# Kernel tuning notes

Measured on AMD Instinct MI355X. Metric: run time of the kernel, lower is better.

## Reference

```python
import jax, jax.numpy as jnp
import numpy as np

B, S, TRG, SRC2 = 64, 2048, 512, 1024  # batch, src_len, trg_hidden, 2*src_hidden


def setup_inputs() -> dict:
    key = jax.random.key(0)
    ks = jax.random.split(key, 9)
    return {
        "dehy": jax.random.normal(ks[0], (B, TRG), dtype=jnp.float32),
        "enhy": jax.random.normal(ks[1], (B, S, SRC2), dtype=jnp.float32),
        "past_attn": jax.random.uniform(ks[2], (B, S), dtype=jnp.float32),
        "src_mask": jax.random.randint(ks[3], (B, S), 0, 2, dtype=jnp.int32),
        # parameters (torch Linear: y = x @ W.T + b)
        "W_en": jax.random.normal(ks[4], (TRG, SRC2), dtype=jnp.float32) * 0.02,
        "b_en": jnp.zeros((TRG,), dtype=jnp.float32),
        "W_de": jax.random.normal(ks[5], (TRG, TRG), dtype=jnp.float32) * 0.02,
        "w_cv": jax.random.normal(ks[6], (TRG,), dtype=jnp.float32) * 0.02,   # attn_cv_in: Linear(1, trg)
        "w_warp": jax.random.normal(ks[7], (TRG,), dtype=jnp.float32) * 0.02, # attn_warp_in: Linear(trg, 1)
    }


def reference(dehy, enhy, past_attn, src_mask, W_en, b_en, W_de, w_cv, w_warp):
    # luong_concat score with 'asee' coverage term
    # attn_agg: [B, S, TRG]
    attn_agg = (
        jnp.einsum("bsd,hd->bsh", enhy, W_en) + b_en
        + (dehy @ W_de.T)[:, None, :]
        + past_attn[..., None] * w_cv
    )
    attn_agg = jnp.tanh(attn_agg)
    attn_ee = jnp.einsum("bsh,h->bs", attn_agg, w_warp)  # [B, S]
    # masked_fill(|mask| == 0, -1e20)
    attn_ee = jnp.where(jnp.abs(src_mask) == 0, jnp.float32(-1e20), attn_ee)
    attn = jax.nn.softmax(attn_ee, axis=1)
    c_encoder = jnp.einsum("bs,bsd->bd", attn, enhy)  # [B, SRC2]
    return (c_encoder, attn, attn_ee)
```

## Files before the change

kernel.cpp:

```cpp
#include <hip/hip_runtime.h>

#define B_   64
#define S_   2048
#define TRG_ 512
#define K_   1024

typedef short short8 __attribute__((ext_vector_type(8)));
typedef float f32x4  __attribute__((ext_vector_type(4)));
typedef unsigned short us4 __attribute__((ext_vector_type(4)));

__device__ __forceinline__ unsigned short f2bf(float f) {
    union { float f; unsigned int u; } v; v.f = f;
    unsigned int u = v.u;
    unsigned int r = (u + 0x7fffu + ((u >> 16) & 1u)) >> 16;
    return (unsigned short)r;
}

__global__ void wen_convert_kernel(const float* __restrict__ Wen,
                                   unsigned short* __restrict__ Wbf) {
    int idx = blockIdx.x * 256 + threadIdx.x;
    float4 f = ((const float4*)Wen)[idx];
    us4 o = { f2bf(f.x), f2bf(f.y), f2bf(f.z), f2bf(f.w) };
    ((us4*)Wbf)[idx] = o;
}

__global__ void deproj_kernel(const float* __restrict__ dehy,
                              const float* __restrict__ Wde,
                              const float* __restrict__ ben,
                              float* __restrict__ dp) {
    int b = blockIdx.x >> 1;
    int h = ((blockIdx.x & 1) << 8) + threadIdx.x;
    const float4* dv = (const float4*)(dehy + (size_t)b * TRG_);
    const float4* wv = (const float4*)(Wde + (size_t)h * TRG_);
    float s = ben[h];
    #pragma unroll 4
    for (int t = 0; t < TRG_ / 4; ++t) {
        float4 a = dv[t], w = wv[t];
        s += a.x * w.x + a.y * w.y + a.z * w.z + a.w * w.w;
    }
    dp[b * TRG_ + h] = s;
}

__global__ __launch_bounds__(512, 2) void score_kernel(
    const float* __restrict__ enhy,
    const unsigned short* __restrict__ Wbf,
    const float* __restrict__ dp,
    const float* __restrict__ past_attn,
    const int* __restrict__ src_mask,
    const float* __restrict__ w_cv,
    const float* __restrict__ w_warp,
    float* __restrict__ out_ee)
{
    __shared__ unsigned short Abuf[2][128 * 32];
    __shared__ unsigned short Bbuf[2][512 * 32];
    __shared__ float red[4][128];

    const int tid  = threadIdx.x;
    const int lane = tid & 63;
    const int w    = tid >> 6;
    const int wm   = w >> 2;
    const int wn   = w & 3;
    const int lj   = lane & 15;
    const int lg   = lane >> 4;
    const int m0   = blockIdx.x * 128;
    const int b    = m0 >> 11;
    const int s0   = m0 & 2047;

    const int kx = ((lg ^ (lane & 3)) << 4);

    f32x4 acc[4][8];
    const f32x4 fz = {0.f, 0.f, 0.f, 0.f};
    #pragma unroll
    for (int i = 0; i < 4; ++i)
        #pragma unroll
        for (int j = 0; j < 8; ++j) acc[i][j] = fz;

    const int arow = tid >> 2;
    const int achk = tid & 3;
    const float* aSrc = enhy + (size_t)(m0 + arow) * K_ + (achk << 3);
    const int aDstByte = arow * 64 + ((achk ^ (arow & 3)) << 4);

    const unsigned short* bSrc[4];
    unsigned short* bDst[4];
    #pragma unroll
    for (int j = 0; j < 4; ++j) {
        int cp = (j << 9) + tid;
        int brow = cp >> 2, bkc = cp & 3;
        bSrc[j] = Wbf + (size_t)brow * K_ + ((bkc ^ (brow & 3)) << 3);
        bDst[j] = &Bbuf[0][0] + ((j << 9) + (w << 6)) * 8;
    }

    float4 a0, a1;
    auto load_a = [&](int kt) {
        const float* p = aSrc + kt * 32;
        a0 = *(const float4*)p;
        a1 = *(const float4*)(p + 4);
    };
    auto write_a = [&](int bufsel) {
        short8 v;
        v[0] = (short)f2bf(a0.x); v[1] = (short)f2bf(a0.y);
        v[2] = (short)f2bf(a0.z); v[3] = (short)f2bf(a0.w);
        v[4] = (short)f2bf(a1.x); v[5] = (short)f2bf(a1.y);
        v[6] = (short)f2bf(a1.z); v[7] = (short)f2bf(a1.w);
        *(short8*)((char*)&Abuf[bufsel][0] + aDstByte) = v;
    };
    auto stage_b = [&](int bufsel, int kt) {
        #pragma unroll
        for (int j = 0; j < 4; ++j) {
            __builtin_amdgcn_global_load_lds(
                (const __attribute__((address_space(1))) void*)(bSrc[j] + kt * 32),
                (__attribute__((address_space(3))) void*)(bDst[j] + bufsel * (512 * 32)),
                16, 0, 0);
        }
    };
    auto compute = [&](int bufsel) {
        const char* Bbase = (const char*)&Bbuf[bufsel][0];
        const char* Abase = (const char*)&Abuf[bufsel][0];
        short8 bf[8];
        #pragma unroll
        for (int fn = 0; fn < 8; ++fn) {
            int r = (wn << 7) + (fn << 4) + lj;
            bf[fn] = *(const short8*)(Bbase + r * 64 + kx);
        }
        #pragma unroll
        for (int fm = 0; fm < 4; ++fm) {
            int rA = (wm << 6) + (fm << 4) + lj;
            short8 af = *(const short8*)(Abase + rA * 64 + kx);
            #pragma unroll
            for (int fn = 0; fn < 8; ++fn)
                acc[fm][fn] = __builtin_amdgcn_mfma_f32_16x16x32_bf16(af, bf[fn], acc[fm][fn], 0, 0, 0);
        }
    };

    load_a(0);
    stage_b(0, 0);
    write_a(0);
    __syncthreads();

    int buf = 0;
    for (int kt = 0; kt < 32; ++kt) {
        if (kt < 31) {
            load_a(kt + 1);
            stage_b(buf ^ 1, kt + 1);
        }
        compute(buf);
        if (kt < 31) write_a(buf ^ 1);
        __syncthreads();
        buf ^= 1;
    }

    float dep[8], wcv8[8], wwp8[8];
    #pragma unroll
    for (int fn = 0; fn < 8; ++fn) {
        int h = (wn << 7) + (fn << 4) + lj;
        dep[fn]  = dp[b * TRG_ + h];
        wcv8[fn] = w_cv[h];
        wwp8[fn] = w_warp[h];
    }
    #pragma unroll
    for (int fm = 0; fm < 4; ++fm) {
        #pragma unroll
        for (int reg = 0; reg < 4; ++reg) {
            int rloc = (wm << 6) + (fm << 4) + (lg << 2) + reg;
            float pa = past_attn[b * S_ + s0 + rloc];
            float p = 0.f;
            #pragma unroll
            for (int fn = 0; fn < 8; ++fn) {
                float v = acc[fm][fn][reg] + dep[fn] + pa * wcv8[fn];
                float e = __expf(2.f * v);
                float t = 1.f - 2.f * __builtin_amdgcn_rcpf(e + 1.f);
                p += t * wwp8[fn];
            }
            p += __shfl_xor(p, 1);
            p += __shfl_xor(p, 2);
            p += __shfl_xor(p, 4);
            p += __shfl_xor(p, 8);
            if (lj == 0) red[wn][rloc] = p;
        }
    }
    __syncthreads();
    if (tid < 128) {
        float ee = red[0][tid] + red[1][tid] + red[2][tid] + red[3][tid];
        int msk = src_mask[b * S_ + s0 + tid];
        if (msk == 0) ee = -1e20f;
        out_ee[m0 + tid] = ee;
    }
}

__global__ void softmax_kernel(const float* __restrict__ ee, float* __restrict__ attn) {
    int b = blockIdx.x, tid = threadIdx.x;
    const float* row = ee + (size_t)b * S_;
    float v[8]; float mx = -3.0e38f;
    #pragma unroll
    for (int i = 0; i < 8; ++i) { v[i] = row[tid + (i << 8)]; mx = fmaxf(mx, v[i]); }
    #pragma unroll
    for (int off = 32; off > 0; off >>= 1) mx = fmaxf(mx, __shfl_xor(mx, off));
    __shared__ float sred[4];
    int w = tid >> 6, lane = tid & 63;
    if (lane == 0) sred[w] = mx;
    __syncthreads();
    mx = fmaxf(fmaxf(sred[0], sred[1]), fmaxf(sred[2], sred[3]));
    float sum = 0.f;
    #pragma unroll
    for (int i = 0; i < 8; ++i) { v[i] = __expf(v[i] - mx); sum += v[i]; }
    #pragma unroll
    for (int off = 32; off > 0; off >>= 1) sum += __shfl_xor(sum, off);
    __syncthreads();
    if (lane == 0) sred[w] = sum;
    __syncthreads();
    sum = sred[0] + sred[1] + sred[2] + sred[3];
    float inv = 1.f / sum;
    float* orow = attn + (size_t)b * S_;
    #pragma unroll
    for (int i = 0; i < 8; ++i) orow[tid + (i << 8)] = v[i] * inv;
}

__global__ void ctx_partial_kernel(const float* __restrict__ attn,
                                   const float* __restrict__ enhy,
                                   float* __restrict__ part) {
    int bx = blockIdx.x;
    int b = bx >> 5, sc = bx & 31;
    int tid = threadIdx.x;
    const float4* e4 = (const float4*)(enhy + ((size_t)b * S_ + sc * 64) * K_);
    const float* ar = attn + (size_t)b * S_ + sc * 64;
    float4 acc = {0.f, 0.f, 0.f, 0.f};
    #pragma unroll 4
    for (int s = 0; s < 64; ++s) {
        float a = ar[s];
        float4 ev = e4[(size_t)s * 256 + tid];
        acc.x += a * ev.x; acc.y += a * ev.y; acc.z += a * ev.z; acc.w += a * ev.w;
    }
    ((float4*)part)[(size_t)(sc * 64 + b) * 256 + tid] = acc;
}

__global__ void ctx_reduce_kernel(const float* __restrict__ part, float* __restrict__ outc) {
    int idx = blockIdx.x * 256 + threadIdx.x;
    int b = idx >> 10, d = idx & 1023;
    float s = 0.f;
    #pragma unroll
    for (int sc = 0; sc < 32; ++sc) s += part[(size_t)((sc << 6) + b) * 1024 + d];
    outc[idx] = s;
}

extern "C" void kernel_launch(void* const* d_in, const int* in_sizes, int n_in,
                              void* d_out, int out_size, void* d_ws, size_t ws_size,
                              hipStream_t stream) {
    (void)in_sizes; (void)n_in; (void)out_size; (void)ws_size;

    const float* dehy = (const float*)d_in[0];
    const float* enhy = (const float*)d_in[1];
    const float* past = (const float*)d_in[2];
    const int*   mask = (const int*)d_in[3];
    const float* Wen  = (const float*)d_in[4];
    const float* ben  = (const float*)d_in[5];
    const float* Wde  = (const float*)d_in[6];
    const float* wcv  = (const float*)d_in[7];
    const float* wwp  = (const float*)d_in[8];

    float* out      = (float*)d_out;
    float* out_c    = out;
    float* out_attn = out + 65536;
    float* out_ee   = out + 65536 + 131072;

    char* ws = (char*)d_ws;
    unsigned short* Wbf = (unsigned short*)ws;
    float* dp   = (float*)(ws + (1 << 20));
    float* part = (float*)(ws + (1 << 20) + (1 << 17));

    wen_convert_kernel<<<512, 256, 0, stream>>>(Wen, Wbf);
    deproj_kernel<<<128, 256, 0, stream>>>(dehy, Wde, ben, dp);
    score_kernel<<<1024, 512, 0, stream>>>(enhy, Wbf, dp, past, mask, wcv, wwp, out_ee);
    softmax_kernel<<<64, 256, 0, stream>>>(out_ee, out_attn);
    ctx_partial_kernel<<<2048, 256, 0, stream>>>(out_attn, enhy, part);
    ctx_reduce_kernel<<<256, 256, 0, stream>>>(part, out_c);
}
```

Baseline: 388.0 us.

## Triple-buffer score GEMM LDS pipeline with explicit waitcnt barriers and new swizzle

Converts the score kernel's double-buffered K loop into a three-stage LDS ring. Global loads for tile kt+2 are issued while tile kt is computed, and each iteration syncs once through explicit vmcnt/lgkmcnt waits and raw s_barrier instead of __syncthreads. It also changes the LDS XOR swizzle to use row>>1, raises MFMA wave priority around the compute block, and unrolls the context partial loop further. The aim is to hide global-load latency and cut LDS bank conflicts. In exchange, shared memory grows to about 123 KB, which may stop two 512-thread blocks fitting per CU, and the hand-counted waitcnts are fragile.

```diff
diff --git a/kernel.cpp b/kernel.cpp
--- a/kernel.cpp
+++ b/kernel.cpp
@@ -51,8 +51,8 @@
     const float* __restrict__ w_warp,
     float* __restrict__ out_ee)
 {
-    __shared__ unsigned short Abuf[2][128 * 32];
-    __shared__ unsigned short Bbuf[2][512 * 32];
+    __shared__ unsigned short Abuf[3][128 * 32];
+    __shared__ unsigned short Bbuf[3][512 * 32];
     __shared__ float red[4][128];
 
     const int tid  = threadIdx.x;
@@ -66,7 +66,7 @@
     const int b    = m0 >> 11;
     const int s0   = m0 & 2047;
 
-    const int kx = ((lg ^ (lane & 3)) << 4);
+    const int kx = ((lg ^ ((lj >> 1) & 3)) << 4);
 
     f32x4 acc[4][8];
     const f32x4 fz = {0.f, 0.f, 0.f, 0.f};
@@ -78,16 +78,16 @@
     const int arow = tid >> 2;
     const int achk = tid & 3;
     const float* aSrc = enhy + (size_t)(m0 + arow) * K_ + (achk << 3);
-    const int aDstByte = arow * 64 + ((achk ^ (arow & 3)) << 4);
+    const int aDstByte = arow * 64 + ((achk ^ ((arow >> 1) & 3)) << 4);
 
     const unsigned short* bSrc[4];
-    unsigned short* bDst[4];
+    int bDstByte[4];
     #pragma unroll
     for (int j = 0; j < 4; ++j) {
         int cp = (j << 9) + tid;
         int brow = cp >> 2, bkc = cp & 3;
-        bSrc[j] = Wbf + (size_t)brow * K_ + ((bkc ^ (brow & 3)) << 3);
-        bDst[j] = &Bbuf[0][0] + ((j << 9) + (w << 6)) * 8;
+        bSrc[j] = Wbf + (size_t)brow * K_ + ((bkc ^ ((brow >> 1) & 3)) << 3);
+        bDstByte[j] = ((j << 9) + (w << 6)) * 16;
     }
 
     float4 a0, a1;
@@ -96,32 +96,33 @@
         a0 = *(const float4*)p;
         a1 = *(const float4*)(p + 4);
     };
-    auto write_a = [&](int bufsel) {
+    auto write_a = [&](int sel) {
         short8 v;
         v[0] = (short)f2bf(a0.x); v[1] = (short)f2bf(a0.y);
         v[2] = (short)f2bf(a0.z); v[3] = (short)f2bf(a0.w);
         v[4] = (short)f2bf(a1.x); v[5] = (short)f2bf(a1.y);
         v[6] = (short)f2bf(a1.z); v[7] = (short)f2bf(a1.w);
-        *(short8*)((char*)&Abuf[bufsel][0] + aDstByte) = v;
-    };
-    auto stage_b = [&](int bufsel, int kt) {
+        *(short8*)((char*)&Abuf[0][0] + sel * 8192 + aDstByte) = v;
+    };
+    auto stage_b = [&](int sel, int kt) {
         #pragma unroll
         for (int j = 0; j < 4; ++j) {
             __builtin_amdgcn_global_load_lds(
                 (const __attribute__((address_space(1))) void*)(bSrc[j] + kt * 32),
-                (__attribute__((address_space(3))) void*)(bDst[j] + bufsel * (512 * 32)),
+                (__attribute__((address_space(3))) void*)((char*)&Bbuf[0][0] + sel * 32768 + bDstByte[j]),
                 16, 0, 0);
         }
     };
-    auto compute = [&](int bufsel) {
-        const char* Bbase = (const char*)&Bbuf[bufsel][0];
-        const char* Abase = (const char*)&Abuf[bufsel][0];
+    auto compute = [&](int sel) {
+        const char* Bbase = (const char*)&Bbuf[0][0] + sel * 32768;
+        const char* Abase = (const char*)&Abuf[0][0] + sel * 8192;
         short8 bf[8];
         #pragma unroll
         for (int fn = 0; fn < 8; ++fn) {
             int r = (wn << 7) + (fn << 4) + lj;
             bf[fn] = *(const short8*)(Bbase + r * 64 + kx);
         }
+        __builtin_amdgcn_s_setprio(1);
         #pragma unroll
         for (int fm = 0; fm < 4; ++fm) {
             int rA = (wm << 6) + (fm << 4) + lj;
@@ -130,24 +131,45 @@
             for (int fn = 0; fn < 8; ++fn)
                 acc[fm][fn] = __builtin_amdgcn_mfma_f32_16x16x32_bf16(af, bf[fn], acc[fm][fn], 0, 0, 0);
         }
+        __builtin_amdgcn_s_setprio(0);
     };
 
     load_a(0);
     stage_b(0, 0);
     write_a(0);
-    __syncthreads();
-
-    int buf = 0;
-    for (int kt = 0; kt < 32; ++kt) {
-        if (kt < 31) {
-            load_a(kt + 1);
-            stage_b(buf ^ 1, kt + 1);
-        }
-        compute(buf);
-        if (kt < 31) write_a(buf ^ 1);
-        __syncthreads();
-        buf ^= 1;
-    }
+    load_a(1);
+    asm volatile("s_waitcnt vmcnt(2)" ::: "memory");
+    asm volatile("s_waitcnt lgkmcnt(0)" ::: "memory");
+    __builtin_amdgcn_sched_barrier(0);
+    __builtin_amdgcn_s_barrier();
+    __builtin_amdgcn_sched_barrier(0);
+    stage_b(1, 1);
+
+    int c0 = 0, c1 = 1, c2 = 2;
+    for (int kt = 0; kt < 30; ++kt) {
+        load_a(kt + 2);
+        write_a(c1);
+        asm volatile("s_waitcnt lgkmcnt(0)" ::: "memory");
+        asm volatile("s_waitcnt vmcnt(6)" ::: "memory");
+        __builtin_amdgcn_sched_barrier(0);
+        __builtin_amdgcn_s_barrier();
+        __builtin_amdgcn_sched_barrier(0);
+        stage_b(c2, kt + 2);
+        compute(c0);
+        int t = c0; c0 = c1; c1 = c2; c2 = t;
+    }
+    write_a(c1);
+    asm volatile("s_waitcnt lgkmcnt(0)" ::: "memory");
+    asm volatile("s_waitcnt vmcnt(4)" ::: "memory");
+    __builtin_amdgcn_sched_barrier(0);
+    __builtin_amdgcn_s_barrier();
+    __builtin_amdgcn_sched_barrier(0);
+    compute(c0);
+    asm volatile("s_waitcnt vmcnt(0)" ::: "memory");
+    __builtin_amdgcn_sched_barrier(0);
+    __builtin_amdgcn_s_barrier();
+    __builtin_amdgcn_sched_barrier(0);
+    compute(c1);
 
     float dep[8], wcv8[8], wwp8[8];
     #pragma unroll
@@ -224,7 +246,7 @@
     const float4* e4 = (const float4*)(enhy + ((size_t)b * S_ + sc * 64) * K_);
     const float* ar = attn + (size_t)b * S_ + sc * 64;
     float4 acc = {0.f, 0.f, 0.f, 0.f};
-    #pragma unroll 4
+    #pragma unroll 8
     for (int s = 0; s < 64; ++s) {
         float a = ar[s];
         float4 ev = e4[(size_t)s * 256 + tid];
```

New measurement: 393.8 us. Within noise of the previous version (+1.5%).

## Replace LDS-staged GEMM in score kernel with direct global-to-register MFMA loads

Applied to the files above, without the earlier changes.

The score kernel stops staging A and B tiles in LDS with double buffering. Each wave now loads its enhy and bf16 W_en fragments straight from global memory into registers and converts A with packed bf16 intrinsics. The block tile drops to 64 rows across all 512 hidden units, so the grid doubles, and occupancy is raised to 4 blocks per CU with a periodic barrier to keep waves in step. This removes LDS traffic and sync overhead, but each of the 8 waves re-reads the same A rows from global/L2 with no LDS reuse, and the per-row converts are repeated per wave. The ctx partial loop unroll is also raised.

```diff
diff --git a/kernel.cpp b/kernel.cpp
--- a/kernel.cpp
+++ b/kernel.cpp
@@ -1,4 +1,5 @@
 #include <hip/hip_runtime.h>
+#include <hip/hip_bf16.h>
 
 #define B_   64
 #define S_   2048
@@ -14,6 +15,15 @@
     unsigned int u = v.u;
     unsigned int r = (u + 0x7fffu + ((u >> 16) & 1u)) >> 16;
     return (unsigned short)r;
+}
+
+__device__ __forceinline__ short8 cvt8(float4 a0, float4 a1) {
+    union { __hip_bfloat162 h[4]; short8 v; } u;
+    u.h[0] = __float22bfloat162_rn(float2{a0.x, a0.y});
+    u.h[1] = __float22bfloat162_rn(float2{a0.z, a0.w});
+    u.h[2] = __float22bfloat162_rn(float2{a1.x, a1.y});
+    u.h[3] = __float22bfloat162_rn(float2{a1.z, a1.w});
+    return u.v;
 }
 
 __global__ void wen_convert_kernel(const float* __restrict__ Wen,
@@ -41,7 +51,7 @@
     dp[b * TRG_ + h] = s;
 }
 
-__global__ __launch_bounds__(512, 2) void score_kernel(
+__global__ __launch_bounds__(512, 4) void score_kernel(
     const float* __restrict__ enhy,
     const unsigned short* __restrict__ Wbf,
     const float* __restrict__ dp,
@@ -51,137 +61,82 @@
     const float* __restrict__ w_warp,
     float* __restrict__ out_ee)
 {
-    __shared__ unsigned short Abuf[2][128 * 32];
-    __shared__ unsigned short Bbuf[2][512 * 32];
-    __shared__ float red[4][128];
+    __shared__ float red[8][64];
 
     const int tid  = threadIdx.x;
     const int lane = tid & 63;
     const int w    = tid >> 6;
-    const int wm   = w >> 2;
-    const int wn   = w & 3;
     const int lj   = lane & 15;
     const int lg   = lane >> 4;
-    const int m0   = blockIdx.x * 128;
+    const int m0   = blockIdx.x * 64;
     const int b    = m0 >> 11;
     const int s0   = m0 & 2047;
 
-    const int kx = ((lg ^ (lane & 3)) << 4);
-
-    f32x4 acc[4][8];
+    f32x4 acc[4][4];
     const f32x4 fz = {0.f, 0.f, 0.f, 0.f};
     #pragma unroll
     for (int i = 0; i < 4; ++i)
         #pragma unroll
-        for (int j = 0; j < 8; ++j) acc[i][j] = fz;
-
-    const int arow = tid >> 2;
-    const int achk = tid & 3;
-    const float* aSrc = enhy + (size_t)(m0 + arow) * K_ + (achk << 3);
-    const int aDstByte = arow * 64 + ((achk ^ (arow & 3)) << 4);
-
-    const unsigned short* bSrc[4];
-    unsigned short* bDst[4];
-    #pragma unroll
-    for (int j = 0; j < 4; ++j) {
-        int cp = (j << 9) + tid;
-        int brow = cp >> 2, bkc = cp & 3;
-        bSrc[j] = Wbf + (size_t)brow * K_ + ((bkc ^ (brow & 3)) << 3);
-        bDst[j] = &Bbuf[0][0] + ((j << 9) + (w << 6)) * 8;
-    }
-
-    float4 a0, a1;
-    auto load_a = [&](int kt) {
-        const float* p = aSrc + kt * 32;
-        a0 = *(const float4*)p;
-        a1 = *(const float4*)(p + 4);
-    };
-    auto write_a = [&](int bufsel) {
-        short8 v;
-        v[0] = (short)f2bf(a0.x); v[1] = (short)f2bf(a0.y);
-        v[2] = (short)f2bf(a0.z); v[3] = (short)f2bf(a0.w);
-        v[4] = (short)f2bf(a1.x); v[5] = (short)f2bf(a1.y);
-        v[6] = (short)f2bf(a1.z); v[7] = (short)f2bf(a1.w);
-        *(short8*)((char*)&Abuf[bufsel][0] + aDstByte) = v;
-    };
-    auto stage_b = [&](int bufsel, int kt) {
-        #pragma unroll
-        for (int j = 0; j < 4; ++j) {
-            __builtin_amdgcn_global_load_lds(
-                (const __attribute__((address_space(1))) void*)(bSrc[j] + kt * 32),
-                (__attribute__((address_space(3))) void*)(bDst[j] + bufsel * (512 * 32)),
-                16, 0, 0);
+        for (int j = 0; j < 4; ++j) acc[i][j] = fz;
+
+    const float* aRow          = enhy + (size_t)(m0 + lj) * K_ + (lg << 3);
+    const unsigned short* bRow = Wbf + (size_t)((w << 6) + lj) * K_ + (lg << 3);
+
+    #pragma unroll 2
+    for (int kt = 0; kt < 32; ++kt) {
+        const int ko = kt << 5;
+        short8 bfr[4];
+        #pragma unroll
+        for (int fn = 0; fn < 4; ++fn)
+            bfr[fn] = *(const short8*)(bRow + (size_t)fn * 16 * K_ + ko);
+        #pragma unroll
+        for (int fm = 0; fm < 4; ++fm) {
+            const float* p = aRow + (size_t)fm * 16 * K_ + ko;
+            float4 a0 = *(const float4*)p;
+            float4 a1 = *(const float4*)(p + 4);
+            short8 af = cvt8(a0, a1);
+            #pragma unroll
+            for (int fn = 0; fn < 4; ++fn)
+                acc[fm][fn] = __builtin_amdgcn_mfma_f32_16x16x32_bf16(af, bfr[fn], acc[fm][fn], 0, 0, 0);
         }
-    };
-    auto compute = [&](int bufsel) {
-        const char* Bbase = (const char*)&Bbuf[bufsel][0];
-        const char* Abase = (const char*)&Abuf[bufsel][0];
-        short8 bf[8];
-        #pragma unroll
-        for (int fn = 0; fn < 8; ++fn) {
-            int r = (wn << 7) + (fn << 4) + lj;
-            bf[fn] = *(const short8*)(Bbase + r * 64 + kx);
-        }
-        #pragma unroll
-        for (int fm = 0; fm < 4; ++fm) {
-            int rA = (wm << 6) + (fm << 4) + lj;
-            short8 af = *(const short8*)(Abase + rA * 64 + kx);
-            #pragma unroll
-            for (int fn = 0; fn < 8; ++fn)
-                acc[fm][fn] = __builtin_amdgcn_mfma_f32_16x16x32_bf16(af, bf[fn], acc[fm][fn], 0, 0, 0);
-        }
-    };
-
-    load_a(0);
-    stage_b(0, 0);
-    write_a(0);
-    __syncthreads();
-
-    int buf = 0;
-    for (int kt = 0; kt < 32; ++kt) {
-        if (kt < 31) {
-            load_a(kt + 1);
-            stage_b(buf ^ 1, kt + 1);
-        }
-        compute(buf);
-        if (kt < 31) write_a(buf ^ 1);
-        __syncthreads();
-        buf ^= 1;
-    }
-
-    float dep[8], wcv8[8], wwp8[8];
-    #pragma unroll
-    for (int fn = 0; fn < 8; ++fn) {
-        int h = (wn << 7) + (fn << 4) + lj;
-        dep[fn]  = dp[b * TRG_ + h];
-        wcv8[fn] = w_cv[h];
-        wwp8[fn] = w_warp[h];
+        if ((kt & 1) == 1) __builtin_amdgcn_s_barrier();
+    }
+
+    float dep4[4], wcv4[4], wwp4[4];
+    #pragma unroll
+    for (int fn = 0; fn < 4; ++fn) {
+        int h = (w << 6) + (fn << 4) + lj;
+        dep4[fn] = dp[b * TRG_ + h];
+        wcv4[fn] = w_cv[h];
+        wwp4[fn] = w_warp[h];
     }
     #pragma unroll
     for (int fm = 0; fm < 4; ++fm) {
         #pragma unroll
         for (int reg = 0; reg < 4; ++reg) {
-            int rloc = (wm << 6) + (fm << 4) + (lg << 2) + reg;
-            float pa = past_attn[b * S_ + s0 + rloc];
+            int row = (fm << 4) + (lg << 2) + reg;
+            float pa = past_attn[b * S_ + s0 + row];
             float p = 0.f;
             #pragma unroll
-            for (int fn = 0; fn < 8; ++fn) {
-                float v = acc[fm][fn][reg] + dep[fn] + pa * wcv8[fn];
+            for (int fn = 0; fn < 4; ++fn) {
+                float v = acc[fm][fn][reg] + dep4[fn] + pa * wcv4[fn];
                 float e = __expf(2.f * v);
                 float t = 1.f - 2.f * __builtin_amdgcn_rcpf(e + 1.f);
-                p += t * wwp8[fn];
+                p += t * wwp4[fn];
             }
             p += __shfl_xor(p, 1);
             p += __shfl_xor(p, 2);
             p += __shfl_xor(p, 4);
             p += __shfl_xor(p, 8);
-            if (lj == 0) red[wn][rloc] = p;
+            if (lj == 0) red[w][row] = p;
         }
     }
     __syncthreads();
-    if (tid < 128) {
-        float ee = red[0][tid] + red[1][tid] + red[2][tid] + red[3][tid];
-        int msk = src_mask[b * S_ + s0 + tid];
+    if (tid < 64) {
+        float ee = 0.f;
+        #pragma unroll
+        for (int ww = 0; ww < 8; ++ww) ee += red[ww][tid];
+        int msk = src_mask[m0 + tid];
         if (msk == 0) ee = -1e20f;
         out_ee[m0 + tid] = ee;
     }
@@ -224,7 +179,7 @@
     const float4* e4 = (const float4*)(enhy + ((size_t)b * S_ + sc * 64) * K_);
     const float* ar = attn + (size_t)b * S_ + sc * 64;
     float4 acc = {0.f, 0.f, 0.f, 0.f};
-    #pragma unroll 4
+    #pragma unroll 8
     for (int s = 0; s < 64; ++s) {
         float a = ar[s];
         float4 ev = e4[(size_t)s * 256 + tid];
@@ -269,7 +224,7 @@
 
     wen_convert_kernel<<<512, 256, 0, stream>>>(Wen, Wbf);
     deproj_kernel<<<128, 256, 0, stream>>>(dehy, Wde, ben, dp);
-    score_kernel<<<1024, 512, 0, stream>>>(enhy, Wbf, dp, past, mask, wcv, wwp, out_ee);
+    score_kernel<<<2048, 512, 0, stream>>>(enhy, Wbf, dp, past, mask, wcv, wwp, out_ee);
     softmax_kernel<<<64, 256, 0, stream>>>(out_ee, out_attn);
     ctx_partial_kernel<<<2048, 256, 0, stream>>>(out_attn, enhy, part);
     ctx_reduce_kernel<<<256, 256, 0, stream>>>(part, out_c);
```

After: 862.2 us. 122% more time.

## Deepen score GEMM pipeline to 4-stage B buffering with register-prefetched A

Applied to the files above, without the earlier changes.

Restructures the score kernel's main loop into a 4-deep LDS ring for the W_en tiles, with A tiles prefetched three steps ahead in registers. Explicit vmcnt waits and raw s_barrier replace the full __syncthreads. It also changes the LDS swizzle, uses packed bf16 conversion intrinsics, raises MFMA wave priority, and unrolls the context partial loop further. The goal is to hide global load latency behind MFMA work. The cost is more LDS (about 144KB per block), which may break the 2-blocks-per-CU launch bound, plus higher register pressure.

```diff
diff --git a/kernel.cpp b/kernel.cpp
--- a/kernel.cpp
+++ b/kernel.cpp
@@ -1,4 +1,5 @@
 #include <hip/hip_runtime.h>
+#include <hip/hip_bf16.h>
 
 #define B_   64
 #define S_   2048
@@ -14,6 +15,15 @@
     unsigned int u = v.u;
     unsigned int r = (u + 0x7fffu + ((u >> 16) & 1u)) >> 16;
     return (unsigned short)r;
+}
+
+__device__ __forceinline__ short8 cvt8(float4 a0, float4 a1) {
+    union { __hip_bfloat162 h[4]; short8 v; } u;
+    u.h[0] = __float22bfloat162_rn(float2{a0.x, a0.y});
+    u.h[1] = __float22bfloat162_rn(float2{a0.z, a0.w});
+    u.h[2] = __float22bfloat162_rn(float2{a1.x, a1.y});
+    u.h[3] = __float22bfloat162_rn(float2{a1.z, a1.w});
+    return u.v;
 }
 
 __global__ void wen_convert_kernel(const float* __restrict__ Wen,
@@ -51,8 +61,8 @@
     const float* __restrict__ w_warp,
     float* __restrict__ out_ee)
 {
+    __shared__ unsigned short Bbuf[4][512 * 32];
     __shared__ unsigned short Abuf[2][128 * 32];
-    __shared__ unsigned short Bbuf[2][512 * 32];
     __shared__ float red[4][128];
 
     const int tid  = threadIdx.x;
@@ -66,7 +76,7 @@
     const int b    = m0 >> 11;
     const int s0   = m0 & 2047;
 
-    const int kx = ((lg ^ (lane & 3)) << 4);
+    const int kx = ((lg ^ ((lj >> 1) & 3)) << 4);
 
     f32x4 acc[4][8];
     const f32x4 fz = {0.f, 0.f, 0.f, 0.f};
@@ -78,76 +88,78 @@
     const int arow = tid >> 2;
     const int achk = tid & 3;
     const float* aSrc = enhy + (size_t)(m0 + arow) * K_ + (achk << 3);
-    const int aDstByte = arow * 64 + ((achk ^ (arow & 3)) << 4);
-
-    const unsigned short* bSrc[4];
-    unsigned short* bDst[4];
-    #pragma unroll
-    for (int j = 0; j < 4; ++j) {
-        int cp = (j << 9) + tid;
-        int brow = cp >> 2, bkc = cp & 3;
-        bSrc[j] = Wbf + (size_t)brow * K_ + ((bkc ^ (brow & 3)) << 3);
-        bDst[j] = &Bbuf[0][0] + ((j << 9) + (w << 6)) * 8;
-    }
-
-    float4 a0, a1;
-    auto load_a = [&](int kt) {
-        const float* p = aSrc + kt * 32;
-        a0 = *(const float4*)p;
-        a1 = *(const float4*)(p + 4);
-    };
-    auto write_a = [&](int bufsel) {
-        short8 v;
-        v[0] = (short)f2bf(a0.x); v[1] = (short)f2bf(a0.y);
-        v[2] = (short)f2bf(a0.z); v[3] = (short)f2bf(a0.w);
-        v[4] = (short)f2bf(a1.x); v[5] = (short)f2bf(a1.y);
-        v[6] = (short)f2bf(a1.z); v[7] = (short)f2bf(a1.w);
-        *(short8*)((char*)&Abuf[bufsel][0] + aDstByte) = v;
-    };
-    auto stage_b = [&](int bufsel, int kt) {
-        #pragma unroll
-        for (int j = 0; j < 4; ++j) {
-            __builtin_amdgcn_global_load_lds(
-                (const __attribute__((address_space(1))) void*)(bSrc[j] + kt * 32),
-                (__attribute__((address_space(3))) void*)(bDst[j] + bufsel * (512 * 32)),
-                16, 0, 0);
-        }
-    };
-    auto compute = [&](int bufsel) {
-        const char* Bbase = (const char*)&Bbuf[bufsel][0];
-        const char* Abase = (const char*)&Abuf[bufsel][0];
-        short8 bf[8];
+    const int aDstByte = arow * 64 + ((achk ^ ((arow >> 1) & 3)) << 4);
+
+    const int brow0 = tid >> 2;
+    const int bkc0  = tid & 3;
+    const unsigned short* bSrc0 = Wbf + (size_t)brow0 * K_ + ((bkc0 ^ ((brow0 >> 1) & 3)) << 3);
+    const int bDst0 = w * 1024;
+
+#define LOADA(R0, R1, kt) { const float* p_ = aSrc + ((kt) << 5); \
+    R0 = *(const float4*)p_; R1 = *(const float4*)(p_ + 4); }
+#define WRITEA(asel, R0, R1) { \
+    *(short8*)((char*)&Abuf[0][0] + (asel) * 8192 + aDstByte) = cvt8(R0, R1); }
+#define STAGEB(bsel, kt) { \
+    _Pragma("unroll") \
+    for (int j_ = 0; j_ < 4; ++j_) { \
+        __builtin_amdgcn_global_load_lds( \
+            (const __attribute__((address_space(1))) void*)(bSrc0 + (size_t)j_ * 128 * K_ + ((kt) << 5)), \
+            (__attribute__((address_space(3))) void*)((char*)&Bbuf[0][0] + (bsel) * 32768 + bDst0 + j_ * 8192), \
+            16, 0, 0); \
+    } }
+#define WAITS(N) \
+    asm volatile("s_waitcnt lgkmcnt(0)" ::: "memory"); \
+    asm volatile("s_waitcnt vmcnt(" #N ")" ::: "memory"); \
+    __builtin_amdgcn_sched_barrier(0); \
+    __builtin_amdgcn_s_barrier(); \
+    __builtin_amdgcn_sched_barrier(0);
+
+    auto compute = [&](int bsel, int asel) {
+        const char* Bbase = (const char*)&Bbuf[0][0] + bsel * 32768;
+        const char* Abase = (const char*)&Abuf[0][0] + asel * 8192;
+        short8 bfr[8];
         #pragma unroll
         for (int fn = 0; fn < 8; ++fn) {
             int r = (wn << 7) + (fn << 4) + lj;
-            bf[fn] = *(const short8*)(Bbase + r * 64 + kx);
+            bfr[fn] = *(const short8*)(Bbase + r * 64 + kx);
         }
+        __builtin_amdgcn_s_setprio(1);
         #pragma unroll
         for (int fm = 0; fm < 4; ++fm) {
             int rA = (wm << 6) + (fm << 4) + lj;
             short8 af = *(const short8*)(Abase + rA * 64 + kx);
             #pragma unroll
             for (int fn = 0; fn < 8; ++fn)
-                acc[fm][fn] = __builtin_amdgcn_mfma_f32_16x16x32_bf16(af, bf[fn], acc[fm][fn], 0, 0, 0);
+                acc[fm][fn] = __builtin_amdgcn_mfma_f32_16x16x32_bf16(af, bfr[fn], acc[fm][fn], 0, 0, 0);
         }
+        __builtin_amdgcn_s_setprio(0);
     };
 
-    load_a(0);
-    stage_b(0, 0);
-    write_a(0);
-    __syncthreads();
-
-    int buf = 0;
-    for (int kt = 0; kt < 32; ++kt) {
-        if (kt < 31) {
-            load_a(kt + 1);
-            stage_b(buf ^ 1, kt + 1);
-        }
-        compute(buf);
-        if (kt < 31) write_a(buf ^ 1);
-        __syncthreads();
-        buf ^= 1;
-    }
+    float4 A0a, A0b, A1a, A1b, A2a, A2b, A3a, A3b;
+
+    LOADA(A0a, A0b, 0);
+    WRITEA(0, A0a, A0b);
+    STAGEB(0, 0);
+    STAGEB(1, 1);
+    LOADA(A1a, A1b, 1);
+    LOADA(A2a, A2b, 2);
+    LOADA(A3a, A3b, 3);
+
+    for (int base = 0; base < 28; base += 4) {
+        WAITS(8) STAGEB(2, base + 2) LOADA(A0a, A0b, base + 4) WRITEA(1, A1a, A1b) compute(0, 0);
+        WAITS(8) STAGEB(3, base + 3) LOADA(A1a, A1b, base + 5) WRITEA(0, A2a, A2b) compute(1, 1);
+        WAITS(8) STAGEB(0, base + 4) LOADA(A2a, A2b, base + 6) WRITEA(1, A3a, A3b) compute(2, 0);
+        WAITS(8) STAGEB(1, base + 5) LOADA(A3a, A3b, base + 7) WRITEA(0, A0a, A0b) compute(3, 1);
+    }
+    WAITS(8) STAGEB(2, 30) WRITEA(1, A1a, A1b) compute(0, 0);
+    WAITS(6) STAGEB(3, 31) WRITEA(0, A2a, A2b) compute(1, 1);
+    WAITS(4)               WRITEA(1, A3a, A3b) compute(2, 0);
+    WAITS(0)                                   compute(3, 1);
+
+#undef LOADA
+#undef WRITEA
+#undef STAGEB
+#undef WAITS
 
     float dep[8], wcv8[8], wwp8[8];
     #pragma unroll
@@ -224,7 +236,7 @@
     const float4* e4 = (const float4*)(enhy + ((size_t)b * S_ + sc * 64) * K_);
     const float* ar = attn + (size_t)b * S_ + sc * 64;
     float4 acc = {0.f, 0.f, 0.f, 0.f};
-    #pragma unroll 4
+    #pragma unroll 8
     for (int s = 0; s < 64; ++s) {
         float a = ar[s];
         float4 ev = e4[(size_t)s * 256 + tid];
```

Result: no change. 385.2 us (-0.7%).
